# Optimization experiments

Hardware: AMD Instinct MI355X
Metric: run time of the kernel (lower is better)

The kernel has to match this reference:

```python
import jax, jax.numpy as jnp
import numpy as np

N, N_H = 256, 64          # detections per image, humans (permuted to top)
NUM_ITER = 2
E = 1024                   # node_encoding_size == box_feature_size
T_LIS, K_LIS, W_LIS = 8.3, 12.0, 10.0


def lis(x):
    # Low-grade Instance Suppression
    return T_LIS / (1.0 + jnp.exp(K_LIS - W_LIS * x))


def setup_inputs() -> dict:
    key = jax.random.key(0)
    ks = jax.random.split(key, 25)
    s = 0.02  # weight scale keeps sigmoid/relu in a sane range
    rn = lambda k, shape, sc=1.0: jax.random.normal(k, shape, jnp.float32) * sc
    inp = {}
    inp['box_features'] = rn(ks[0], (N, 12544))            # [N, 256*7*7]
    inp['node_spatial'] = rn(ks[1], (N, 1024))             # conv spatial-head output
    inp['scores'] = jax.random.uniform(ks[2], (N,), jnp.float32)
    labels = jax.random.randint(ks[3], (N,), 1, 80)
    inp['labels'] = labels.at[:N_H].set(0)                 # humans (idx 0) on top
    inp['class_mask'] = jax.random.bernoulli(ks[4], 0.2, (80, 117))
    inp['W_bh1'] = rn(ks[5], (12544, 1024), s); inp['b_bh1'] = jnp.zeros((1024,), jnp.float32)
    inp['W_bh2'] = rn(ks[6], (1024, 1024), s);  inp['b_bh2'] = jnp.zeros((1024,), jnp.float32)
    inp['W_sa']  = rn(ks[7], (1024, 1024), s)
    inp['W_a1']  = rn(ks[8], (4096, 2048), s); inp['b_a1'] = jnp.zeros((2048,), jnp.float32)
    inp['W_a2']  = rn(ks[9], (2048, 1024), s); inp['b_a2'] = jnp.zeros((1024,), jnp.float32)
    inp['W_a3']  = rn(ks[10], (1024, 1), s);   inp['b_a3'] = jnp.zeros((1,), jnp.float32)
    inp['W_hm']  = rn(ks[11], (1024, 1024), s); inp['b_hm'] = jnp.zeros((1024,), jnp.float32)
    inp['W_om']  = rn(ks[12], (1024, 1024), s); inp['b_om'] = jnp.zeros((1024,), jnp.float32)
    inp['W_hu']  = rn(ks[13], (2048, 1024), s)
    inp['W_ou']  = rn(ks[14], (2048, 1024), s)
    return inp


def _keep_indices():
    xv, yv = np.meshgrid(np.arange(N_H), np.arange(N), indexing='ij')
    m = (xv != yv).ravel()
    return jnp.asarray(xv.ravel()[m]), jnp.asarray(yv.ravel()[m])


def reference(box_features, node_spatial, scores, W_bh1, b_bh1, W_bh2, b_bh2,
              W_sa, W_a1, b_a1, W_a2, b_a2, W_a3, b_a3,
              W_hm, b_hm, W_om, b_om, W_hu, W_ou, labels, class_mask):
    # box_head: Flatten -> Linear -> ReLU -> Linear -> ReLU
    enc = jax.nn.relu(box_features @ W_bh1 + b_bh1)
    enc = jax.nn.relu(enc @ W_bh2 + b_bh2)                 # [N, E]
    h_enc = enc[:N_H]                                      # [N_H, E]
    h_sp = node_spatial[:N_H]                              # [N_H, 1024]
    # spatial_attention on pairwise spatial differences (fixed across iters)
    diff = node_spatial[None, :, :] - h_sp[:, None, :]     # [N_H, N, 1024]
    h_to_o = jnp.einsum('hnd,de->hne', diff, W_sa)         # Linear, no bias
    o_to_h = -h_to_o
    adj = jnp.ones((N_H, N), enc.dtype)
    for _ in range(NUM_ITER):
        # adjacency MLP + sigmoid over all n_h*n pairs
        hf = jnp.concatenate([h_enc, h_sp], axis=1)        # [N_H, 2048]
        of = jnp.concatenate([enc, node_spatial], axis=1)  # [N, 2048]
        pair_in = jnp.concatenate([
            jnp.broadcast_to(hf[:, None, :], (N_H, N, 2 * E)),
            jnp.broadcast_to(of[None, :, :], (N_H, N, 2 * E))], axis=-1)  # [N_H,N,4096]
        hdn = jax.nn.relu(pair_in @ W_a1 + b_a1)
        hdn = jax.nn.relu(hdn @ W_a2 + b_a2)
        adj = jax.nn.sigmoid((hdn @ W_a3 + b_a3)[..., 0])  # [N_H, N]
        # object -> human messages
        obj_msg = jax.nn.relu(enc @ W_om + b_om)           # [N, R]
        agg_o = (adj[..., None] * (obj_msg[None, :, :] * o_to_h)).sum(1)  # [N_H, R]
        h_enc = jnp.concatenate([h_enc, agg_o], axis=1) @ W_hu            # [N_H, E]
        # human -> object messages
        hum_msg = jax.nn.relu(h_enc @ W_hm + b_hm)         # [N_H, R]
        agg_h = (adj[..., None] * (hum_msg[:, None, :] * h_to_o)).sum(0)  # [N, R]
        enc = jnp.concatenate([enc, agg_h], axis=1) @ W_ou                # [N, E]
    x_keep, y_keep = _keep_indices()                       # [P], P = N_H*N - N_H
    pair_feats = jnp.concatenate([h_enc[x_keep], h_sp[x_keep],
                                  enc[y_keep], node_spatial[y_keep]], axis=1)  # [P, 4096]
    # prior scores: LIS(score_h)*LIS(score_o) scattered to valid target classes
    prod = lis(scores[x_keep]) * lis(scores[y_keep])       # [P]
    prior = prod[:, None] * class_mask[labels[y_keep]].astype(pair_feats.dtype)  # [P, 117]
    prior = adj[x_keep, y_keep][:, None] * prior
    return jnp.concatenate([pair_feats, prior], axis=1)    # [P, 4096+117]
```

## Files before the change

kernel.cpp:

```cpp
#include <hip/hip_runtime.h>

using bf16 = __bf16;
typedef __bf16 bf16x4 __attribute__((ext_vector_type(4)));
typedef __bf16 bf16x8 __attribute__((ext_vector_type(8)));
typedef float  f32x4  __attribute__((ext_vector_type(4)));

#define GST 40

__device__ __forceinline__ float ldf(const void* p, size_t i, int f32) {
    return f32 ? ((const float*)p)[i] : (float)((const bf16*)p)[i];
}
__device__ __forceinline__ bf16x8 ld8(const void* p, size_t i, int f32) {
    bf16x8 r;
    if (f32) {
        f32x4 a = *(const f32x4*)((const float*)p + i);
        f32x4 b = *(const f32x4*)((const float*)p + i + 4);
#pragma unroll
        for (int j = 0; j < 4; ++j) { r[j] = (bf16)a[j]; r[j + 4] = (bf16)b[j]; }
    } else {
        r = *(const bf16x8*)((const bf16*)p + i);
    }
    return r;
}
__device__ __forceinline__ void st1(void* p, size_t i, float v, int f32) {
    if (f32) ((float*)p)[i] = v;
    else     ((bf16*)p)[i] = (bf16)v;
}

__device__ __forceinline__ void gl_lds16(const bf16* g, bf16* l) {
    __builtin_amdgcn_global_load_lds(
        (const __attribute__((address_space(1))) void*)g,
        (__attribute__((address_space(3))) void*)l, 16, 0, 0);
}

__global__ void init_flag(int* __restrict__ dflag) { *dflag = 0; }

__global__ void detect_kernel(const unsigned short* __restrict__ p, int n,
                              int* __restrict__ dflag)
{
    const unsigned int* q = (const unsigned int*)p;
    const int nw = n >> 1;
    int hit = 0;
    for (int i = blockIdx.x * 256 + threadIdx.x; i < nw; i += gridDim.x * 256) {
        unsigned int w = q[i];
        if ((w & 0x7F80u) == 0x7F80u || (w & 0x7F800000u) == 0x7F800000u) hit = 1;
    }
    if (__any(hit) && (threadIdx.x & 63) == 0) atomicOr(dflag, 1);
}

__global__ void cvt_kernel(const void* __restrict__ src, bf16* __restrict__ dst,
                           int n, const int* __restrict__ dflag)
{
    const int f32 = *dflag;
    const int stride = gridDim.x * 256;
    const int nv = n >> 3;
    for (int i = blockIdx.x * 256 + threadIdx.x; i < nv; i += stride) {
        bf16x8 v = ld8(src, (size_t)i * 8, f32);
        *(bf16x8*)(dst + (size_t)i * 8) = v;
    }
}

__global__ void cvt_smalls(const void* b_bh1, const void* b_bh2, const void* b_om,
                           const void* b_hm, const void* b_a1, const void* b_a2,
                           const void* w_a3, const void* b_a3, const void* scores,
                           bf16* __restrict__ smalls, const int* __restrict__ dflag)
{
    const int f32 = *dflag;
    int i = blockIdx.x * 256 + threadIdx.x;
    const void* s; int off;
    if      (i < 1024) { s = b_bh1; off = 0;    }
    else if (i < 2048) { s = b_bh2; off = 1024; }
    else if (i < 3072) { s = b_om;  off = 2048; }
    else if (i < 4096) { s = b_hm;  off = 3072; }
    else if (i < 6144) { s = b_a1;  off = 4096; }
    else if (i < 7168) { s = b_a2;  off = 6144; }
    else if (i < 8192) { s = w_a3;  off = 7168; }
    else if (i < 8193) { s = b_a3;  off = 8192; }
    else if (i >= 8208 && i < 8464) { s = scores; off = 8208; }
    else return;
    smalls[i] = (bf16)ldf(s, i - off, f32);
}

__global__ void transpose_any(const void* __restrict__ W, bf16* __restrict__ Wt,
                              int K, int N, const int* __restrict__ dflag)
{
    __shared__ bf16 tile[32][33];
    const int f32 = *dflag;
    const int n0 = blockIdx.x * 32, k0 = blockIdx.y * 32;
    const int tx = threadIdx.x, ty = threadIdx.y;
#pragma unroll
    for (int i = 0; i < 4; ++i)
        tile[ty + i * 8][tx] = (bf16)ldf(W, (size_t)(k0 + ty + i * 8) * N + n0 + tx, f32);
    __syncthreads();
#pragma unroll
    for (int i = 0; i < 4; ++i)
        Wt[(size_t)(n0 + ty + i * 8) * K + k0 + tx] = tile[tx][ty + i * 8];
}

__global__ __launch_bounds__(256)
void gemm_p(const bf16* __restrict__ A, int lda,
            const void* __restrict__ B, size_t boff, int ldb,
            float* __restrict__ part, int N, int Kc,
            const int* __restrict__ dflag)
{
    __shared__ bf16 As[64 * GST];
    __shared__ bf16 Bs[64 * GST];
    const int f32 = *dflag;
    const int t = threadIdx.x;
    const int l = t & 63;
    const int quad = l >> 4, lr = l & 15;
    const int w = t >> 6, wm = w >> 1, wn = w & 1;
    const int mBlock = blockIdx.y * 64, nBlock = blockIdx.x * 64;
    const int ar = t >> 2, ac = (t & 3) * 8;
    const int kr = t >> 3, nc = (t & 7) * 8;
    const int kBeg = blockIdx.z * Kc;
    const int nIter = Kc >> 5;

    f32x4 acc[2][2] = {};

    bf16x8 avr = *(const bf16x8*)(A + (size_t)(mBlock + ar) * lda + kBeg + ac);
    bf16x8 bvr = ld8(B, boff + (size_t)(kBeg + kr) * ldb + nBlock + nc, f32);

    for (int it = 0; it < nIter; ++it) {
        *(bf16x8*)&As[ar * GST + ac] = avr;
#pragma unroll
        for (int j = 0; j < 8; ++j) {
            int wr = nc + j;
            Bs[wr * GST + (kr ^ (((wr >> 3) & 3) << 3))] = bvr[j];
        }
        __syncthreads();
        if (it + 1 < nIter) {
            int k0 = kBeg + (it + 1) * 32;
            avr = *(const bf16x8*)(A + (size_t)(mBlock + ar) * lda + k0 + ac);
            bvr = ld8(B, boff + (size_t)(k0 + kr) * ldb + nBlock + nc, f32);
        }
        bf16x8 af[2], bfr[2];
#pragma unroll
        for (int mi = 0; mi < 2; ++mi)
            af[mi] = *(const bf16x8*)&As[(wm * 32 + mi * 16 + lr) * GST + quad * 8];
#pragma unroll
        for (int nj = 0; nj < 2; ++nj) {
            int row = wn * 32 + nj * 16 + lr;
            bfr[nj] = *(const bf16x8*)&Bs[row * GST + ((quad * 8) ^ (((row >> 3) & 3) << 3))];
        }
#pragma unroll
        for (int mi = 0; mi < 2; ++mi)
#pragma unroll
            for (int nj = 0; nj < 2; ++nj)
                acc[mi][nj] = __builtin_amdgcn_mfma_f32_16x16x32_bf16(
                    af[mi], bfr[nj], acc[mi][nj], 0, 0, 0);
        __syncthreads();
    }

    float* outp = part + (size_t)blockIdx.z * ((size_t)gridDim.y * 64 * N);
#pragma unroll
    for (int mi = 0; mi < 2; ++mi)
#pragma unroll
        for (int nj = 0; nj < 2; ++nj) {
            int col = nBlock + wn * 32 + nj * 16 + lr;
#pragma unroll
            for (int rr = 0; rr < 4; ++rr) {
                int row = mBlock + wm * 32 + mi * 16 + quad * 4 + rr;
                outp[(size_t)row * N + col] = acc[mi][nj][rr];
            }
        }
}

template<bool RELU, bool BIAS, bool F32OUT>
__global__ void reduce_k(const float* __restrict__ part, int S, int total,
                         const bf16* __restrict__ bias, void* __restrict__ out,
                         int N, int ldd)
{
    int base = (blockIdx.x * 256 + threadIdx.x) * 4;
    if (base >= total) return;
    f32x4 s = *(const f32x4*)(part + base);
    for (int z = 1; z < S; ++z) {
        f32x4 v = *(const f32x4*)(part + (size_t)z * total + base);
        s[0] += v[0]; s[1] += v[1]; s[2] += v[2]; s[3] += v[3];
    }
    int row = base / N, col = base % N;
    size_t ob = (size_t)row * ldd + col;
#pragma unroll
    for (int j = 0; j < 4; ++j) {
        float v = s[j];
        if (BIAS) v += (float)bias[col + j];
        if (RELU) v = fmaxf(v, 0.f);
        if (F32OUT) ((float*)out)[ob + j] = v;
        else        ((bf16*)out)[ob + j] = (bf16)v;
    }
}

__global__ void build_pairA(const float* __restrict__ Hb, const float* __restrict__ Op,
                            bf16* __restrict__ A)
{
    const int n = blockIdx.x;
    const int h = blockIdx.y;
    const int k = threadIdx.x * 8;
    const float* hp = Hb + (size_t)h * 2048 + k;
    const float* op = Op + (size_t)n * 2048 + k;
    f32x4 h0 = *(const f32x4*)hp, h1 = *(const f32x4*)(hp + 4);
    f32x4 o0 = *(const f32x4*)op, o1 = *(const f32x4*)(op + 4);
    bf16x8 r;
#pragma unroll
    for (int j = 0; j < 4; ++j) {
        r[j]     = (bf16)fmaxf(h0[j] + o0[j], 0.f);
        r[j + 4] = (bf16)fmaxf(h1[j] + o1[j], 0.f);
    }
    *(bf16x8*)(A + ((size_t)h * 256 + n) * 2048 + k) = r;
}

__global__ __launch_bounds__(256)
void pair_gemm(const bf16* __restrict__ Apg, const bf16* __restrict__ Wt_a2,
               const bf16* __restrict__ b_a2, const bf16* __restrict__ w_a3,
               float* __restrict__ slots)
{
    __shared__ bf16 As[2][128 * 32];
    __shared__ bf16 Bs[2][128 * 32];
    const int t = threadIdx.x;
    const int l = t & 63, w = t >> 6;
    const int quad = l >> 4, lr = l & 15;
    const int wm = w >> 1, wn = w & 1;
    const int nb = blockIdx.y & 7;
    const int mb = blockIdx.x * 16 + (blockIdx.y >> 3);
    const int p0 = mb * 128;

    const int grow = w * 16 + (l >> 2);
    const int slot = l & 3;
    const int csrc = slot ^ ((grow >> 1) & 3);
    const bf16* Asrc0 = Apg + (size_t)(p0 + grow) * 2048 + csrc * 8;
    const bf16* Asrc1 = Apg + (size_t)(p0 + 64 + grow) * 2048 + csrc * 8;
    const bf16* Bsrc0 = Wt_a2 + (size_t)(nb * 128 + grow) * 2048 + csrc * 8;
    const bf16* Bsrc1 = Wt_a2 + (size_t)(nb * 128 + 64 + grow) * 2048 + csrc * 8;
    const int woff = w * 512;

    f32x4 acc[4][4] = {};

    gl_lds16(Asrc0, As[0] + woff);
    gl_lds16(Asrc1, As[0] + 2048 + woff);
    gl_lds16(Bsrc0, Bs[0] + woff);
    gl_lds16(Bsrc1, Bs[0] + 2048 + woff);
    __syncthreads();

    int cur = 0;
    for (int kt = 0; kt < 64; ++kt) {
        if (kt < 63) {
            int kn = (kt + 1) * 32;
            bf16* An = As[cur ^ 1];
            bf16* Bn = Bs[cur ^ 1];
            gl_lds16(Asrc0 + kn, An + woff);
            gl_lds16(Asrc1 + kn, An + 2048 + woff);
            gl_lds16(Bsrc0 + kn, Bn + woff);
            gl_lds16(Bsrc1 + kn, Bn + 2048 + woff);
        }
        const bf16* Ac = As[cur];
        const bf16* Bc = Bs[cur];
        bf16x8 af[4], bfr[4];
#pragma unroll
        for (int mi = 0; mi < 4; ++mi) {
            int row = wm * 64 + mi * 16 + lr;
            int sl = quad ^ ((row >> 1) & 3);
            af[mi] = *(const bf16x8*)&Ac[row * 32 + sl * 8];
        }
#pragma unroll
        for (int nj = 0; nj < 4; ++nj) {
            int row = wn * 64 + nj * 16 + lr;
            int sl = quad ^ ((row >> 1) & 3);
            bfr[nj] = *(const bf16x8*)&Bc[row * 32 + sl * 8];
        }
#pragma unroll
        for (int mi = 0; mi < 4; ++mi)
#pragma unroll
            for (int nj = 0; nj < 4; ++nj)
                acc[mi][nj] = __builtin_amdgcn_mfma_f32_16x16x32_bf16(
                    af[mi], bfr[nj], acc[mi][nj], 0, 0, 0);
        __syncthreads();
        cur ^= 1;
    }

    float w3v[4], b2v[4];
#pragma unroll
    for (int nj = 0; nj < 4; ++nj) {
        int col = nb * 128 + wn * 64 + nj * 16 + lr;
        w3v[nj] = (float)w_a3[col];
        b2v[nj] = (float)b_a2[col];
    }
#pragma unroll
    for (int mi = 0; mi < 4; ++mi) {
        f32x4 rs = {0.f, 0.f, 0.f, 0.f};
#pragma unroll
        for (int nj = 0; nj < 4; ++nj)
#pragma unroll
            for (int rr = 0; rr < 4; ++rr)
                rs[rr] += fmaxf(acc[mi][nj][rr] + b2v[nj], 0.f) * w3v[nj];
#pragma unroll
        for (int off = 1; off < 16; off <<= 1) {
            rs[0] += __shfl_xor(rs[0], off);
            rs[1] += __shfl_xor(rs[1], off);
            rs[2] += __shfl_xor(rs[2], off);
            rs[3] += __shfl_xor(rs[3], off);
        }
        if (lr == 0) {
            int p = p0 + wm * 64 + mi * 16 + quad * 4;
            int slot2 = nb * 2 + wn;
            slots[(size_t)(p + 0) * 16 + slot2] = rs[0];
            slots[(size_t)(p + 1) * 16 + slot2] = rs[1];
            slots[(size_t)(p + 2) * 16 + slot2] = rs[2];
            slots[(size_t)(p + 3) * 16 + slot2] = rs[3];
        }
    }
}

__global__ void adj_finalize(const float* __restrict__ slots,
                             const bf16* __restrict__ b_a3, float* __restrict__ adj)
{
    int i = blockIdx.x * 256 + threadIdx.x;
    float s = (float)b_a3[0];
#pragma unroll
    for (int k = 0; k < 16; ++k) s += slots[(size_t)i * 16 + k];
    adj[i] = 1.f / (1.f + expf(-s));
}

__global__ void copy_rows(const bf16* __restrict__ src, int lds_,
                          bf16* __restrict__ dst, int ldd)
{
    int c = blockIdx.x * 256 + threadIdx.x;
    int r = blockIdx.y;
    dst[(size_t)r * ldd + c] = src[(size_t)r * lds_ + c];
}

__global__ void agg_o_kernel(const float* __restrict__ adj, const bf16* __restrict__ obj_msg,
                             const bf16* __restrict__ nsW, const bf16* __restrict__ hf,
                             bf16* __restrict__ out)
{
    int bx = blockIdx.x;
    int h = blockIdx.y;
    int e = (bx & 3) * 256 + threadIdx.x;
    if (bx < 4) {
        out[(size_t)h * 2048 + e] = hf[(size_t)h * 2048 + e];
        return;
    }
    float nh = (float)nsW[h * 1024 + e];
    float s = 0.f;
    for (int n = 0; n < 256; ++n) {
        float a  = adj[h * 256 + n];
        float om = (float)obj_msg[n * 1024 + e];
        float nw = (float)nsW[n * 1024 + e];
        s += a * om * (nh - nw);
    }
    out[(size_t)h * 2048 + 1024 + e] = (bf16)s;
}

__global__ void agg_h_kernel(const float* __restrict__ adj, const bf16* __restrict__ hum_msg,
                             const bf16* __restrict__ nsW, const bf16* __restrict__ of,
                             bf16* __restrict__ out)
{
    int bx = blockIdx.x;
    int n = blockIdx.y;
    int e = (bx & 3) * 256 + threadIdx.x;
    if (bx < 4) {
        out[(size_t)n * 2048 + e] = of[(size_t)n * 2048 + e];
        return;
    }
    float nn = (float)nsW[n * 1024 + e];
    float s = 0.f;
    for (int h = 0; h < 64; ++h) {
        float a  = adj[h * 256 + n];
        float hm = (float)hum_msg[h * 1024 + e];
        float nw = (float)nsW[h * 1024 + e];
        s += a * hm * (nn - nw);
    }
    out[(size_t)n * 2048 + 1024 + e] = (bf16)s;
}

__global__ void out_kernel(const bf16* __restrict__ hf, const bf16* __restrict__ of,
                           const bf16* __restrict__ nsp_bf, const float* __restrict__ adj,
                           const bf16* __restrict__ scores_bf, const int* __restrict__ labels,
                           const int* __restrict__ cmask, void* __restrict__ out,
                           const int* __restrict__ dflag)
{
    const int f32 = *dflag;
    const int r = blockIdx.x;
    const int x = r / 255;
    const int tt = r % 255;
    const int y = tt + (tt >= x ? 1 : 0);
    const size_t rbase = (size_t)r * 4213;
    const bf16* seg[4] = { hf + (size_t)x * 2048, nsp_bf + x * 1024,
                           of + (size_t)y * 2048, nsp_bf + y * 1024 };
    const int t = threadIdx.x;

    float sx = (float)scores_bf[x], sy = (float)scores_bf[y];
    float lx = 8.3f / (1.f + expf(12.f - 10.f * sx));
    float ly = 8.3f / (1.f + expf(12.f - 10.f * sy));
    float pf = adj[x * 256 + y] * lx * ly;
    const int* cm = cmask + labels[y] * 117;

    auto getv = [&](int e) -> float {
        if (e < 4096) return (float)seg[e >> 10][e & 1023];
        return cm[e - 4096] ? pf : 0.f;
    };

    if (f32) {
        float* op = (float*)out + rbase;
        const int ali = (int)((4 - (rbase & 3)) & 3);
        const int nv = (4213 - ali) >> 2;
        for (int vi = t; vi < nv; vi += 256) {
            int e0 = ali + vi * 4;
            f32x4 v = { getv(e0), getv(e0 + 1), getv(e0 + 2), getv(e0 + 3) };
            *(f32x4*)(op + e0) = v;
        }
        if (t < ali) op[t] = getv(t);
        int te = ali + nv * 4;
        if (t < 4213 - te) op[te + t] = getv(te + t);
    } else {
        bf16* op = (bf16*)out + rbase;
        for (int e = t; e < 4213; e += 256) op[e] = (bf16)getv(e);
    }
}

extern "C" void kernel_launch(void* const* d_in, const int* in_sizes, int n_in,
                              void* d_out, int out_size, void* d_ws, size_t ws_size,
                              hipStream_t stream)
{
    (void)in_sizes; (void)n_in; (void)out_size; (void)ws_size;
    const void* box    = d_in[0];
    const void* nsp    = d_in[1];
    const void* scores = d_in[2];
    const int*  labels = (const int*)d_in[3];
    const int*  cmask  = (const int*)d_in[4];
    const void* W_bh1 = d_in[5],  *b_bh1 = d_in[6];
    const void* W_bh2 = d_in[7],  *b_bh2 = d_in[8];
    const void* W_sa  = d_in[9];
    const void* W_a1  = d_in[10], *b_a1  = d_in[11];
    const void* W_a2  = d_in[12], *b_a2  = d_in[13];
    const void* W_a3  = d_in[14], *b_a3  = d_in[15];
    const void* W_hm  = d_in[16], *b_hm  = d_in[17];
    const void* W_om  = d_in[18], *b_om  = d_in[19];
    const void* W_hu  = d_in[20];
    const void* W_ou  = d_in[21];

    char* ws = (char*)d_ws;
    size_t off = 0;
    auto alloc = [&](size_t bytes) -> void* {
        off = (off + 255) & ~(size_t)255;
        void* p = ws + off;
        off += bytes;
        return p;
    };
    int*  dflag   = (int*)alloc(4);
    bf16* box_bf  = (bf16*)alloc((size_t)256 * 12544 * 2);
    bf16* nsp_bf  = (bf16*)alloc((size_t)256 * 1024 * 2);
    bf16* Wt_a2   = (bf16*)alloc((size_t)1024 * 2048 * 2);
    bf16* smalls  = (bf16*)alloc((size_t)8464 * 2);
    bf16* sb_bh1 = smalls,        *sb_bh2 = smalls + 1024;
    bf16* sb_om  = smalls + 2048, *sb_hm  = smalls + 3072;
    bf16* sb_a1  = smalls + 4096, *sb_a2  = smalls + 6144;
    bf16* sw_a3  = smalls + 7168, *sb_a3  = smalls + 8192;
    bf16* sscore = smalls + 8208;
    bf16* t0      = (bf16*)alloc((size_t)256 * 1024 * 2);
    bf16* nsW     = (bf16*)alloc((size_t)256 * 1024 * 2);
    bf16* hf      = (bf16*)alloc((size_t)64 * 2048 * 2);
    bf16* of      = (bf16*)alloc((size_t)256 * 2048 * 2);
    float* Hpart  = (float*)alloc((size_t)64 * 2048 * 4);
    float* Opart  = (float*)alloc((size_t)256 * 2048 * 4);
    float* slots  = (float*)alloc((size_t)16384 * 16 * 4);
    float* adj    = (float*)alloc((size_t)16384 * 4);
    bf16* obj_msg = (bf16*)alloc((size_t)256 * 1024 * 2);
    bf16* hu_in   = (bf16*)alloc((size_t)64 * 2048 * 2);
    bf16* hum_msg = (bf16*)alloc((size_t)64 * 1024 * 2);
    bf16* ou_in   = (bf16*)alloc((size_t)256 * 2048 * 2);
    float* part   = (float*)alloc((size_t)2097152 * 4);
    bf16* A_bf    = (bf16*)alloc((size_t)16384 * 2048 * 2);

    init_flag<<<1, 1, 0, stream>>>(dflag);
    detect_kernel<<<256, 256, 0, stream>>>((const unsigned short*)box, 524288, dflag);

    cvt_kernel<<<1568, 256, 0, stream>>>(box, box_bf, 256 * 12544, dflag);
    cvt_kernel<<<128, 256, 0, stream>>>(nsp, nsp_bf, 256 * 1024, dflag);
    cvt_smalls<<<34, 256, 0, stream>>>(b_bh1, b_bh2, b_om, b_hm, b_a1, b_a2,
                                       W_a3, b_a3, scores, smalls, dflag);

    transpose_any<<<dim3(1024 / 32, 2048 / 32), dim3(32, 8), 0, stream>>>(
        W_a2, Wt_a2, 2048, 1024, dflag);

    gemm_p<<<dim3(16, 4, 8), 256, 0, stream>>>(box_bf, 12544, W_bh1, 0, 1024, part, 1024, 1568, dflag);
    reduce_k<true, true, false><<<dim3(256), 256, 0, stream>>>(part, 8, 262144, sb_bh1, t0, 1024, 1024);
    gemm_p<<<dim3(16, 4, 4), 256, 0, stream>>>(t0, 1024, W_bh2, 0, 1024, part, 1024, 256, dflag);
    reduce_k<true, true, false><<<dim3(256), 256, 0, stream>>>(part, 4, 262144, sb_bh2, of, 1024, 2048);
    gemm_p<<<dim3(16, 4, 4), 256, 0, stream>>>(nsp_bf, 1024, W_sa, 0, 1024, part, 1024, 256, dflag);
    reduce_k<false, false, false><<<dim3(256), 256, 0, stream>>>(part, 4, 262144, nullptr, nsW, 1024, 1024);
    copy_rows<<<dim3(4, 64), 256, 0, stream>>>(of, 2048, hf, 2048);
    copy_rows<<<dim3(4, 64), 256, 0, stream>>>(nsp_bf, 1024, hf + 1024, 2048);
    copy_rows<<<dim3(4, 256), 256, 0, stream>>>(nsp_bf, 1024, of + 1024, 2048);

    for (int it = 0; it < 2; ++it) {
        gemm_p<<<dim3(32, 1, 8), 256, 0, stream>>>(hf, 2048, W_a1, 0, 2048, part, 2048, 256, dflag);
        reduce_k<false, true, true><<<dim3(128), 256, 0, stream>>>(part, 8, 131072, sb_a1, Hpart, 2048, 2048);
        gemm_p<<<dim3(32, 4, 4), 256, 0, stream>>>(of, 2048, W_a1, (size_t)2048 * 2048, 2048, part, 2048, 512, dflag);
        reduce_k<false, false, true><<<dim3(512), 256, 0, stream>>>(part, 4, 524288, nullptr, Opart, 2048, 2048);
        build_pairA<<<dim3(256, 64), 256, 0, stream>>>(Hpart, Opart, A_bf);
        pair_gemm<<<dim3(8, 128), 256, 0, stream>>>(A_bf, Wt_a2, sb_a2, sw_a3, slots);
        adj_finalize<<<dim3(64), 256, 0, stream>>>(slots, sb_a3, adj);
        gemm_p<<<dim3(16, 4, 4), 256, 0, stream>>>(of, 2048, W_om, 0, 1024, part, 1024, 256, dflag);
        reduce_k<true, true, false><<<dim3(256), 256, 0, stream>>>(part, 4, 262144, sb_om, obj_msg, 1024, 1024);
        agg_o_kernel<<<dim3(8, 64), 256, 0, stream>>>(adj, obj_msg, nsW, hf, hu_in);
        gemm_p<<<dim3(16, 1, 16), 256, 0, stream>>>(hu_in, 2048, W_hu, 0, 1024, part, 1024, 128, dflag);
        reduce_k<false, false, false><<<dim3(64), 256, 0, stream>>>(part, 16, 65536, nullptr, hf, 1024, 2048);
        gemm_p<<<dim3(16, 1, 16), 256, 0, stream>>>(hf, 2048, W_hm, 0, 1024, part, 1024, 64, dflag);
        reduce_k<true, true, false><<<dim3(64), 256, 0, stream>>>(part, 16, 65536, sb_hm, hum_msg, 1024, 1024);
        agg_h_kernel<<<dim3(8, 256), 256, 0, stream>>>(adj, hum_msg, nsW, of, ou_in);
        gemm_p<<<dim3(16, 4, 4), 256, 0, stream>>>(ou_in, 2048, W_ou, 0, 1024, part, 1024, 512, dflag);
        reduce_k<false, false, false><<<dim3(256), 256, 0, stream>>>(part, 4, 262144, nullptr, of, 1024, 2048);
    }

    out_kernel<<<dim3(16320), 256, 0, stream>>>(
        hf, of, nsp_bf, adj, sscore, labels, cmask, d_out, dflag);
}
```

Baseline: 966.1 us.

## Double-buffer gemm_p shared tiles and fuse setup conversion/copy launches

The split-K GEMM now keeps two LDS buffers, so the next tile is stored into the alternate buffer after the MFMAs and only one barrier is needed per K step instead of two. The three input-conversion kernels are merged into a single launch, and the three row-copy kernels are merged into one concat kernel. The aim is to cut barrier stalls in every GEMM and remove launch overhead, at the cost of doubling the LDS footprint of gemm_p.

```diff
diff --git a/kernel.cpp b/kernel.cpp
--- a/kernel.cpp
+++ b/kernel.cpp
@@ -48,25 +48,29 @@
     if (__any(hit) && (threadIdx.x & 63) == 0) atomicOr(dflag, 1);
 }
 
-__global__ void cvt_kernel(const void* __restrict__ src, bf16* __restrict__ dst,
-                           int n, const int* __restrict__ dflag)
-{
-    const int f32 = *dflag;
-    const int stride = gridDim.x * 256;
-    const int nv = n >> 3;
-    for (int i = blockIdx.x * 256 + threadIdx.x; i < nv; i += stride) {
-        bf16x8 v = ld8(src, (size_t)i * 8, f32);
-        *(bf16x8*)(dst + (size_t)i * 8) = v;
-    }
-}
-
-__global__ void cvt_smalls(const void* b_bh1, const void* b_bh2, const void* b_om,
-                           const void* b_hm, const void* b_a1, const void* b_a2,
-                           const void* w_a3, const void* b_a3, const void* scores,
-                           bf16* __restrict__ smalls, const int* __restrict__ dflag)
+#define CVT_V1 401408
+#define CVT_V2 32768
+__global__ void cvt_fused(const void* __restrict__ box, bf16* __restrict__ box_bf,
+                          const void* __restrict__ nsp, bf16* __restrict__ nsp_bf,
+                          const void* b_bh1, const void* b_bh2, const void* b_om,
+                          const void* b_hm, const void* b_a1, const void* b_a2,
+                          const void* w_a3, const void* b_a3, const void* scores,
+                          bf16* __restrict__ smalls, const int* __restrict__ dflag)
 {
     const int f32 = *dflag;
     int i = blockIdx.x * 256 + threadIdx.x;
+    if (i < CVT_V1) {
+        bf16x8 v = ld8(box, (size_t)i * 8, f32);
+        *(bf16x8*)(box_bf + (size_t)i * 8) = v;
+        return;
+    }
+    i -= CVT_V1;
+    if (i < CVT_V2) {
+        bf16x8 v = ld8(nsp, (size_t)i * 8, f32);
+        *(bf16x8*)(nsp_bf + (size_t)i * 8) = v;
+        return;
+    }
+    i -= CVT_V2;
     const void* s; int off;
     if      (i < 1024) { s = b_bh1; off = 0;    }
     else if (i < 2048) { s = b_bh2; off = 1024; }
@@ -103,8 +107,8 @@
             float* __restrict__ part, int N, int Kc,
             const int* __restrict__ dflag)
 {
-    __shared__ bf16 As[64 * GST];
-    __shared__ bf16 Bs[64 * GST];
+    __shared__ bf16 As[2][64 * GST];
+    __shared__ bf16 Bs[2][64 * GST];
     const int f32 = *dflag;
     const int t = threadIdx.x;
     const int l = t & 63;
@@ -118,30 +122,37 @@
 
     f32x4 acc[2][2] = {};
 
-    bf16x8 avr = *(const bf16x8*)(A + (size_t)(mBlock + ar) * lda + kBeg + ac);
-    bf16x8 bvr = ld8(B, boff + (size_t)(kBeg + kr) * ldb + nBlock + nc, f32);
-
-    for (int it = 0; it < nIter; ++it) {
-        *(bf16x8*)&As[ar * GST + ac] = avr;
+    {
+        bf16x8 avr = *(const bf16x8*)(A + (size_t)(mBlock + ar) * lda + kBeg + ac);
+        bf16x8 bvr = ld8(B, boff + (size_t)(kBeg + kr) * ldb + nBlock + nc, f32);
+        *(bf16x8*)&As[0][ar * GST + ac] = avr;
 #pragma unroll
         for (int j = 0; j < 8; ++j) {
             int wr = nc + j;
-            Bs[wr * GST + (kr ^ (((wr >> 3) & 3) << 3))] = bvr[j];
-        }
-        __syncthreads();
-        if (it + 1 < nIter) {
+            Bs[0][wr * GST + (kr ^ (((wr >> 3) & 3) << 3))] = bvr[j];
+        }
+    }
+    __syncthreads();
+
+    int cur = 0;
+    for (int it = 0; it < nIter; ++it) {
+        const bool more = (it + 1 < nIter);
+        bf16x8 av2, bv2;
+        if (more) {
             int k0 = kBeg + (it + 1) * 32;
-            avr = *(const bf16x8*)(A + (size_t)(mBlock + ar) * lda + k0 + ac);
-            bvr = ld8(B, boff + (size_t)(k0 + kr) * ldb + nBlock + nc, f32);
-        }
+            av2 = *(const bf16x8*)(A + (size_t)(mBlock + ar) * lda + k0 + ac);
+            bv2 = ld8(B, boff + (size_t)(k0 + kr) * ldb + nBlock + nc, f32);
+        }
+        const bf16* Ac = As[cur];
+        const bf16* Bc = Bs[cur];
         bf16x8 af[2], bfr[2];
 #pragma unroll
         for (int mi = 0; mi < 2; ++mi)
-            af[mi] = *(const bf16x8*)&As[(wm * 32 + mi * 16 + lr) * GST + quad * 8];
+            af[mi] = *(const bf16x8*)&Ac[(wm * 32 + mi * 16 + lr) * GST + quad * 8];
 #pragma unroll
         for (int nj = 0; nj < 2; ++nj) {
             int row = wn * 32 + nj * 16 + lr;
-            bfr[nj] = *(const bf16x8*)&Bs[row * GST + ((quad * 8) ^ (((row >> 3) & 3) << 3))];
+            bfr[nj] = *(const bf16x8*)&Bc[row * GST + ((quad * 8) ^ (((row >> 3) & 3) << 3))];
         }
 #pragma unroll
         for (int mi = 0; mi < 2; ++mi)
@@ -149,7 +160,18 @@
             for (int nj = 0; nj < 2; ++nj)
                 acc[mi][nj] = __builtin_amdgcn_mfma_f32_16x16x32_bf16(
                     af[mi], bfr[nj], acc[mi][nj], 0, 0, 0);
+        if (more) {
+            bf16* An = As[cur ^ 1];
+            bf16* Bn = Bs[cur ^ 1];
+            *(bf16x8*)&An[ar * GST + ac] = av2;
+#pragma unroll
+            for (int j = 0; j < 8; ++j) {
+                int wr = nc + j;
+                Bn[wr * GST + (kr ^ (((wr >> 3) & 3) << 3))] = bv2[j];
+            }
+        }
         __syncthreads();
+        cur ^= 1;
     }
 
     float* outp = part + (size_t)blockIdx.z * ((size_t)gridDim.y * 64 * N);
@@ -320,12 +342,20 @@
     adj[i] = 1.f / (1.f + expf(-s));
 }
 
-__global__ void copy_rows(const bf16* __restrict__ src, int lds_,
-                          bf16* __restrict__ dst, int ldd)
+__global__ void setup_concat(const bf16* __restrict__ nsp_bf, const bf16* __restrict__ of_ro,
+                             bf16* __restrict__ of, bf16* __restrict__ hf)
 {
     int c = blockIdx.x * 256 + threadIdx.x;
     int r = blockIdx.y;
-    dst[(size_t)r * ldd + c] = src[(size_t)r * lds_ + c];
+    if (r < 256) {
+        of[(size_t)r * 2048 + 1024 + c] = nsp_bf[(size_t)r * 1024 + c];
+    } else if (r < 320) {
+        int rr = r - 256;
+        hf[(size_t)rr * 2048 + 1024 + c] = nsp_bf[(size_t)rr * 1024 + c];
+    } else {
+        int rr = r - 320;
+        hf[(size_t)rr * 2048 + c] = of_ro[(size_t)rr * 2048 + c];
+    }
 }
 
 __global__ void agg_o_kernel(const float* __restrict__ adj, const bf16* __restrict__ obj_msg,
@@ -474,10 +504,9 @@
     init_flag<<<1, 1, 0, stream>>>(dflag);
     detect_kernel<<<256, 256, 0, stream>>>((const unsigned short*)box, 524288, dflag);
 
-    cvt_kernel<<<1568, 256, 0, stream>>>(box, box_bf, 256 * 12544, dflag);
-    cvt_kernel<<<128, 256, 0, stream>>>(nsp, nsp_bf, 256 * 1024, dflag);
-    cvt_smalls<<<34, 256, 0, stream>>>(b_bh1, b_bh2, b_om, b_hm, b_a1, b_a2,
-                                       W_a3, b_a3, scores, smalls, dflag);
+    cvt_fused<<<(CVT_V1 + CVT_V2 + 8464 + 255) / 256, 256, 0, stream>>>(
+        box, box_bf, nsp, nsp_bf, b_bh1, b_bh2, b_om, b_hm, b_a1, b_a2,
+        W_a3, b_a3, scores, smalls, dflag);
 
     transpose_any<<<dim3(1024 / 32, 2048 / 32), dim3(32, 8), 0, stream>>>(
         W_a2, Wt_a2, 2048, 1024, dflag);
@@ -488,9 +517,7 @@
     reduce_k<true, true, false><<<dim3(256), 256, 0, stream>>>(part, 4, 262144, sb_bh2, of, 1024, 2048);
     gemm_p<<<dim3(16, 4, 4), 256, 0, stream>>>(nsp_bf, 1024, W_sa, 0, 1024, part, 1024, 256, dflag);
     reduce_k<false, false, false><<<dim3(256), 256, 0, stream>>>(part, 4, 262144, nullptr, nsW, 1024, 1024);
-    copy_rows<<<dim3(4, 64), 256, 0, stream>>>(of, 2048, hf, 2048);
-    copy_rows<<<dim3(4, 64), 256, 0, stream>>>(nsp_bf, 1024, hf + 1024, 2048);
-    copy_rows<<<dim3(4, 256), 256, 0, stream>>>(nsp_bf, 1024, of + 1024, 2048);
+    setup_concat<<<dim3(4, 384), 256, 0, stream>>>(nsp_bf, of, of, hf);
 
     for (int it = 0; it < 2; ++it) {
         gemm_p<<<dim3(32, 1, 8), 256, 0, stream>>>(hf, 2048, W_a1, 0, 2048, part, 2048, 256, dflag);
```

Measured after the change: 964.4 us. No clear change (-0.2%).
